# Kernel optimization log

Hardware: AMD Instinct MI355X
Metric: run time of the kernel (lower is better)

Reference implementation:

```python
import jax, jax.numpy as jnp
import numpy as np

B, L, CIN, COUT = 8, 2048, 1024, 1024


def setup_inputs() -> dict:
    key = jax.random.key(0)
    ks = jax.random.split(key, 13)
    s_in = 1.0 / np.sqrt(CIN)
    s_out = 1.0 / np.sqrt(COUT)
    return {
        "query": jax.random.normal(ks[0], (B, L, CIN), jnp.float32),
        "key": jax.random.normal(ks[1], (B, L, CIN), jnp.float32),
        "value": jax.random.normal(ks[2], (B, L, CIN), jnp.float32),
        "Wq": jax.random.uniform(ks[3], (COUT, CIN), jnp.float32, -s_in, s_in),
        "bq": jax.random.uniform(ks[4], (COUT,), jnp.float32, -s_in, s_in),
        "Wk": jax.random.uniform(ks[5], (COUT, CIN), jnp.float32, -s_in, s_in),
        "bk": jax.random.uniform(ks[6], (COUT,), jnp.float32, -s_in, s_in),
        "Wv": jax.random.uniform(ks[7], (COUT, CIN), jnp.float32, -s_in, s_in),
        "bv": jax.random.uniform(ks[8], (COUT,), jnp.float32, -s_in, s_in),
        "fcq_w": jax.random.uniform(ks[9], (1, COUT), jnp.float32, -s_out, s_out),
        "fcq_b": jax.random.uniform(ks[10], (1,), jnp.float32, -s_out, s_out),
        "fck_w": jax.random.uniform(ks[11], (1, COUT), jnp.float32, -s_out, s_out),
        "fck_b": jax.random.uniform(ks[12], (1,), jnp.float32, -s_out, s_out),
    }


def reference(query, key, value, Wq, bq, Wk, bk, Wv, bv, fcq_w, fcq_b, fck_w, fck_b):
    # Linear projections (torch Linear: x @ W^T + b)
    w_query = jnp.einsum('blc,oc->blo', query, Wq) + bq   # [B, Lq, COUT]
    w_key = jnp.einsum('blc,oc->blo', key, Wk) + bk       # [B, Lk, COUT]
    w_value = jnp.einsum('blc,oc->blo', value, Wv) + bv   # [B, Lk, COUT]
    # Scalar scores per position, then outer-sum -> [B, Lq, Lk]
    fc_query = jnp.einsum('blo,xo->blx', w_query, fcq_w) + fcq_b  # [B, Lq, 1]
    fc_key = jnp.einsum('blo,xo->blx', w_key, fck_w) + fck_b      # [B, Lk, 1]
    attns = fc_query + jnp.swapaxes(fc_key, 1, 2)                 # [B, Lq, Lk]
    attns = jax.nn.softmax(attns, axis=-1)
    # dropout p=0.0 (eval) -> identity
    outputs = jnp.einsum('bqk,bkd->bqd', attns, w_value)          # [B, Lq, COUT]
    # note: original applies activation to attns after bmm but discards it
    return outputs
```

## Files before the change

kernel.cpp:

```cpp
#include <hip/hip_runtime.h>

#define CIN  1024
#define COUT 1024
#define LB   2048
#define BB   8


__global__ __launch_bounds__(256) void k_u(const float* __restrict__ Wk,
                                           const float* __restrict__ fckw,
                                           float* __restrict__ u) {
    __shared__ float4 red[256];
    const float4* Wk4 = (const float4*)Wk;
    int t = threadIdx.x;
    int cc = blockIdx.x & 3;
    int oc = blockIdx.x >> 2;
    int c4 = cc * 64 + (t & 63);
    int w  = t >> 6;
    float4 acc = make_float4(0.f, 0.f, 0.f, 0.f);
    #pragma unroll
    for (int j = 0; j < 16; ++j) {
        int o = oc * 64 + w + j * 4;
        float f = fckw[o];
        float4 a = Wk4[(size_t)o * 256 + c4];
        acc.x += f * a.x; acc.y += f * a.y; acc.z += f * a.z; acc.w += f * a.w;
    }
    red[t] = acc;
    __syncthreads();
    if (t < 64) {
        float4 a = red[t], b = red[t + 64], c = red[t + 128], d = red[t + 192];
        float4 s;
        s.x = a.x + b.x + c.x + d.x;
        s.y = a.y + b.y + c.y + d.y;
        s.z = a.z + b.z + c.z + d.z;
        s.w = a.w + b.w + c.w + d.w;
        float* up = u + (size_t)cc * 256 + t * 4;
        atomicAdd(up + 0, s.x);
        atomicAdd(up + 1, s.y);
        atomicAdd(up + 2, s.z);
        atomicAdd(up + 3, s.w);
    }
}

__global__ __launch_bounds__(256) void k_scores(const float* __restrict__ key,
                                                const float* __restrict__ u,
                                                float* __restrict__ s) {
    __shared__ float su[CIN];
    int tid = threadIdx.x;
    ((float4*)su)[tid] = ((const float4*)u)[tid];
    __syncthreads();
    int wave = tid >> 6, lane = tid & 63;
    int r = blockIdx.x * 4 + wave;
    const float4* row = (const float4*)(key + (size_t)r * CIN);
    const float4* su4 = (const float4*)su;
    float acc = 0.f;
    #pragma unroll
    for (int j = 0; j < 4; ++j) {
        float4 a = row[lane + j * 64];
        float4 b = su4[lane + j * 64];
        acc += a.x * b.x + a.y * b.y + a.z * b.z + a.w * b.w;
    }
    #pragma unroll
    for (int off = 32; off; off >>= 1) acc += __shfl_down(acc, off, 64);
    if (lane == 0) s[r] = acc;
}

__global__ __launch_bounds__(256) void k_softmax(const float* __restrict__ s,
                                                 float* __restrict__ p,
                                                 float* __restrict__ vbar) {
    __shared__ float wred[4];
    int b = blockIdx.x, t = threadIdx.x;
    int wave = t >> 6, lane = t & 63;
    const float4* s4 = (const float4*)(s + (size_t)b * LB);
    float4 v0 = s4[t], v1 = s4[t + 256];
    float m = fmaxf(fmaxf(fmaxf(v0.x, v0.y), fmaxf(v0.z, v0.w)),
                    fmaxf(fmaxf(v1.x, v1.y), fmaxf(v1.z, v1.w)));
    #pragma unroll
    for (int off = 32; off; off >>= 1) m = fmaxf(m, __shfl_down(m, off, 64));
    if (lane == 0) wred[wave] = m;
    __syncthreads();
    m = fmaxf(fmaxf(wred[0], wred[1]), fmaxf(wred[2], wred[3]));
    __syncthreads();
    v0.x = __expf(v0.x - m); v0.y = __expf(v0.y - m);
    v0.z = __expf(v0.z - m); v0.w = __expf(v0.w - m);
    v1.x = __expf(v1.x - m); v1.y = __expf(v1.y - m);
    v1.z = __expf(v1.z - m); v1.w = __expf(v1.w - m);
    float sum = v0.x + v0.y + v0.z + v0.w + v1.x + v1.y + v1.z + v1.w;
    #pragma unroll
    for (int off = 32; off; off >>= 1) sum += __shfl_down(sum, off, 64);
    if (lane == 0) wred[wave] = sum;
    __syncthreads();
    float inv = 1.f / (wred[0] + wred[1] + wred[2] + wred[3]);
    v0.x *= inv; v0.y *= inv; v0.z *= inv; v0.w *= inv;
    v1.x *= inv; v1.y *= inv; v1.z *= inv; v1.w *= inv;
    float4* p4 = (float4*)(p + (size_t)b * LB);
    p4[t] = v0; p4[t + 256] = v1;
    ((float4*)(vbar + (size_t)b * CIN))[t] = make_float4(0.f, 0.f, 0.f, 0.f);
}

__global__ __launch_bounds__(256) void k_vbar(const float* __restrict__ value,
                                              const float* __restrict__ p,
                                              float* __restrict__ vbar) {
    __shared__ float pl[32];
    int t = threadIdx.x;
    int b  = blockIdx.x >> 6;
    int k0 = (blockIdx.x & 63) * 32;
    if (t < 32) pl[t] = p[(size_t)b * LB + k0 + t];
    __syncthreads();
    const float4* v4 = (const float4*)value + ((size_t)b * LB + k0) * 256 + t;
    float4 acc = make_float4(0.f, 0.f, 0.f, 0.f);
    #pragma unroll 8
    for (int k = 0; k < 32; ++k) {
        float pw = pl[k];
        float4 a = v4[(size_t)k * 256];
        acc.x += pw * a.x; acc.y += pw * a.y; acc.z += pw * a.z; acc.w += pw * a.w;
    }
    float* vp = vbar + (size_t)b * CIN + t * 4;
    atomicAdd(vp + 0, acc.x);
    atomicAdd(vp + 1, acc.y);
    atomicAdd(vp + 2, acc.z);
    atomicAdd(vp + 3, acc.w);
}

__global__ __launch_bounds__(256) void k_orow(const float* __restrict__ Wv,
                                              const float* __restrict__ bv,
                                              const float* __restrict__ vbar,
                                              float* __restrict__ orow) {
    __shared__ float sv[CIN];
    int tid = threadIdx.x;
    int r0 = blockIdx.x * 4;
    int b = r0 >> 10;
    ((float4*)sv)[tid] = ((const float4*)(vbar + (size_t)b * CIN))[tid];
    __syncthreads();
    int wave = tid >> 6, lane = tid & 63;
    int r = r0 + wave;
    int d = r & 1023;
    const float4* row = (const float4*)(Wv + (size_t)d * CIN);
    const float4* sv4 = (const float4*)sv;
    float acc = 0.f;
    #pragma unroll
    for (int j = 0; j < 4; ++j) {
        float4 a = row[lane + j * 64];
        float4 v = sv4[lane + j * 64];
        acc += a.x * v.x + a.y * v.y + a.z * v.z + a.w * v.w;
    }
    #pragma unroll
    for (int off = 32; off; off >>= 1) acc += __shfl_down(acc, off, 64);
    if (lane == 0) orow[r] = acc + bv[d];
}

__global__ __launch_bounds__(256) void k_bcast(const float* __restrict__ orow,
                                               float* __restrict__ out) {
    int t = threadIdx.x;
    int b  = blockIdx.x >> 8;
    int q0 = (blockIdx.x & 255) * 8;
    float4 val = ((const float4*)orow)[b * 256 + t];
    float4* out4 = (float4*)out;
    #pragma unroll
    for (int j = 0; j < 8; ++j)
        out4[((size_t)b * LB + q0 + j) * 256 + t] = val;
}

extern "C" void kernel_launch(void* const* d_in, const int* in_sizes, int n_in,
                              void* d_out, int out_size, void* d_ws, size_t ws_size,
                              hipStream_t stream) {
    const float* key   = (const float*)d_in[1];
    const float* value = (const float*)d_in[2];
    const float* Wk    = (const float*)d_in[5];
    const float* Wv    = (const float*)d_in[7];
    const float* bv    = (const float*)d_in[8];
    const float* fckw  = (const float*)d_in[11];

    float* ws   = (float*)d_ws;
    float* u    = ws;
    float* s    = ws + 1024;
    float* p    = ws + 17408;
    float* vbar = ws + 33792;
    float* orow = ws + 41984;
    float* out  = (float*)d_out;

    hipMemsetAsync(u, 0, 1024 * sizeof(float), stream);

    hipLaunchKernelGGL(k_u,       dim3(64),   dim3(256), 0, stream, Wk, fckw, u);
    hipLaunchKernelGGL(k_scores,  dim3(4096), dim3(256), 0, stream, key, u, s);
    hipLaunchKernelGGL(k_softmax, dim3(8),    dim3(256), 0, stream, s, p, vbar);
    hipLaunchKernelGGL(k_vbar,    dim3(512),  dim3(256), 0, stream, value, p, vbar);
    hipLaunchKernelGGL(k_orow,    dim3(2048), dim3(256), 0, stream, Wv, bv, vbar, orow);
    hipLaunchKernelGGL(k_bcast,   dim3(2048), dim3(256), 0, stream, orow, out);
}
```

Baseline: 242.4 us.

## Fuse key scoring, exponentiation and value weighting into one kernel

Merges the score, softmax and weighted-value kernels into a single pass. Each block computes scores for 16 key rows, exponentiates them and immediately accumulates exp-weighted value rows. It keeps an unnormalised numerator and a denominator with atomics, and divides by the denominator inside the output-row kernel. This removes two launches, the tiny 8-block softmax kernel and the round trips of the score and probability buffers. In exchange it drops the max subtraction, so exp overflow is possible if the scores are large.

```diff
diff --git a/kernel.cpp b/kernel.cpp
--- a/kernel.cpp
+++ b/kernel.cpp
@@ -41,95 +41,76 @@
     }
 }
 
-__global__ __launch_bounds__(256) void k_scores(const float* __restrict__ key,
-                                                const float* __restrict__ u,
-                                                float* __restrict__ s) {
+__global__ __launch_bounds__(256) void k_fused(const float* __restrict__ key,
+                                               const float* __restrict__ value,
+                                               const float* __restrict__ u,
+                                               float* __restrict__ num,
+                                               float* __restrict__ den) {
     __shared__ float su[CIN];
-    int tid = threadIdx.x;
-    ((float4*)su)[tid] = ((const float4*)u)[tid];
+    __shared__ float4 sacc[4][256];
+    __shared__ float sden[4];
+    int t = threadIdx.x;
+    ((float4*)su)[t] = ((const float4*)u)[t];
     __syncthreads();
-    int wave = tid >> 6, lane = tid & 63;
-    int r = blockIdx.x * 4 + wave;
-    const float4* row = (const float4*)(key + (size_t)r * CIN);
+    int wave = t >> 6, lane = t & 63;
+    int b  = blockIdx.x >> 7;
+    int k0 = (blockIdx.x & 127) * 16;
     const float4* su4 = (const float4*)su;
-    float acc = 0.f;
+    float4 acc0 = make_float4(0,0,0,0), acc1 = acc0, acc2 = acc0, acc3 = acc0;
+    float dsum = 0.f;
     #pragma unroll
     for (int j = 0; j < 4; ++j) {
-        float4 a = row[lane + j * 64];
-        float4 b = su4[lane + j * 64];
-        acc += a.x * b.x + a.y * b.y + a.z * b.z + a.w * b.w;
+        int k = k0 + j * 4 + wave;
+        const float4* krow = (const float4*)(key + ((size_t)b * LB + k) * CIN);
+        float s = 0.f;
+        #pragma unroll
+        for (int seg = 0; seg < 4; ++seg) {
+            float4 a = krow[lane + seg * 64];
+            float4 uu = su4[lane + seg * 64];
+            s += a.x * uu.x + a.y * uu.y + a.z * uu.z + a.w * uu.w;
+        }
+        #pragma unroll
+        for (int off = 32; off; off >>= 1) s += __shfl_down(s, off, 64);
+        float e = __expf(__shfl(s, 0, 64));
+        dsum += e;
+        const float4* vrow = (const float4*)(value + ((size_t)b * LB + k) * CIN);
+        float4 a;
+        a = vrow[lane];       acc0.x += e*a.x; acc0.y += e*a.y; acc0.z += e*a.z; acc0.w += e*a.w;
+        a = vrow[lane + 64];  acc1.x += e*a.x; acc1.y += e*a.y; acc1.z += e*a.z; acc1.w += e*a.w;
+        a = vrow[lane + 128]; acc2.x += e*a.x; acc2.y += e*a.y; acc2.z += e*a.z; acc2.w += e*a.w;
+        a = vrow[lane + 192]; acc3.x += e*a.x; acc3.y += e*a.y; acc3.z += e*a.z; acc3.w += e*a.w;
     }
-    #pragma unroll
-    for (int off = 32; off; off >>= 1) acc += __shfl_down(acc, off, 64);
-    if (lane == 0) s[r] = acc;
-}
-
-__global__ __launch_bounds__(256) void k_softmax(const float* __restrict__ s,
-                                                 float* __restrict__ p,
-                                                 float* __restrict__ vbar) {
-    __shared__ float wred[4];
-    int b = blockIdx.x, t = threadIdx.x;
-    int wave = t >> 6, lane = t & 63;
-    const float4* s4 = (const float4*)(s + (size_t)b * LB);
-    float4 v0 = s4[t], v1 = s4[t + 256];
-    float m = fmaxf(fmaxf(fmaxf(v0.x, v0.y), fmaxf(v0.z, v0.w)),
-                    fmaxf(fmaxf(v1.x, v1.y), fmaxf(v1.z, v1.w)));
-    #pragma unroll
-    for (int off = 32; off; off >>= 1) m = fmaxf(m, __shfl_down(m, off, 64));
-    if (lane == 0) wred[wave] = m;
+    sacc[wave][lane]       = acc0;
+    sacc[wave][lane + 64]  = acc1;
+    sacc[wave][lane + 128] = acc2;
+    sacc[wave][lane + 192] = acc3;
+    if (lane == 0) sden[wave] = dsum;
     __syncthreads();
-    m = fmaxf(fmaxf(wred[0], wred[1]), fmaxf(wred[2], wred[3]));
-    __syncthreads();
-    v0.x = __expf(v0.x - m); v0.y = __expf(v0.y - m);
-    v0.z = __expf(v0.z - m); v0.w = __expf(v0.w - m);
-    v1.x = __expf(v1.x - m); v1.y = __expf(v1.y - m);
-    v1.z = __expf(v1.z - m); v1.w = __expf(v1.w - m);
-    float sum = v0.x + v0.y + v0.z + v0.w + v1.x + v1.y + v1.z + v1.w;
-    #pragma unroll
-    for (int off = 32; off; off >>= 1) sum += __shfl_down(sum, off, 64);
-    if (lane == 0) wred[wave] = sum;
-    __syncthreads();
-    float inv = 1.f / (wred[0] + wred[1] + wred[2] + wred[3]);
-    v0.x *= inv; v0.y *= inv; v0.z *= inv; v0.w *= inv;
-    v1.x *= inv; v1.y *= inv; v1.z *= inv; v1.w *= inv;
-    float4* p4 = (float4*)(p + (size_t)b * LB);
-    p4[t] = v0; p4[t + 256] = v1;
-    ((float4*)(vbar + (size_t)b * CIN))[t] = make_float4(0.f, 0.f, 0.f, 0.f);
-}
-
-__global__ __launch_bounds__(256) void k_vbar(const float* __restrict__ value,
-                                              const float* __restrict__ p,
-                                              float* __restrict__ vbar) {
-    __shared__ float pl[32];
-    int t = threadIdx.x;
-    int b  = blockIdx.x >> 6;
-    int k0 = (blockIdx.x & 63) * 32;
-    if (t < 32) pl[t] = p[(size_t)b * LB + k0 + t];
-    __syncthreads();
-    const float4* v4 = (const float4*)value + ((size_t)b * LB + k0) * 256 + t;
-    float4 acc = make_float4(0.f, 0.f, 0.f, 0.f);
-    #pragma unroll 8
-    for (int k = 0; k < 32; ++k) {
-        float pw = pl[k];
-        float4 a = v4[(size_t)k * 256];
-        acc.x += pw * a.x; acc.y += pw * a.y; acc.z += pw * a.z; acc.w += pw * a.w;
-    }
-    float* vp = vbar + (size_t)b * CIN + t * 4;
-    atomicAdd(vp + 0, acc.x);
-    atomicAdd(vp + 1, acc.y);
-    atomicAdd(vp + 2, acc.z);
-    atomicAdd(vp + 3, acc.w);
+    float4 a0 = sacc[0][t], a1 = sacc[1][t], a2 = sacc[2][t], a3 = sacc[3][t];
+    float4 s4;
+    s4.x = a0.x + a1.x + a2.x + a3.x;
+    s4.y = a0.y + a1.y + a2.y + a3.y;
+    s4.z = a0.z + a1.z + a2.z + a3.z;
+    s4.w = a0.w + a1.w + a2.w + a3.w;
+    int c = (t >> 6) * 256 + (t & 63) * 4;
+    float* np = num + (size_t)b * CIN + c;
+    atomicAdd(np + 0, s4.x);
+    atomicAdd(np + 1, s4.y);
+    atomicAdd(np + 2, s4.z);
+    atomicAdd(np + 3, s4.w);
+    if (t == 0) atomicAdd(&den[b], sden[0] + sden[1] + sden[2] + sden[3]);
 }
 
 __global__ __launch_bounds__(256) void k_orow(const float* __restrict__ Wv,
                                               const float* __restrict__ bv,
-                                              const float* __restrict__ vbar,
+                                              const float* __restrict__ num,
+                                              const float* __restrict__ den,
                                               float* __restrict__ orow) {
     __shared__ float sv[CIN];
     int tid = threadIdx.x;
     int r0 = blockIdx.x * 4;
     int b = r0 >> 10;
-    ((float4*)sv)[tid] = ((const float4*)(vbar + (size_t)b * CIN))[tid];
+    ((float4*)sv)[tid] = ((const float4*)(num + (size_t)b * CIN))[tid];
     __syncthreads();
     int wave = tid >> 6, lane = tid & 63;
     int r = r0 + wave;
@@ -145,7 +126,7 @@
     }
     #pragma unroll
     for (int off = 32; off; off >>= 1) acc += __shfl_down(acc, off, 64);
-    if (lane == 0) orow[r] = acc + bv[d];
+    if (lane == 0) orow[r] = acc / den[b] + bv[d];
 }
 
 __global__ __launch_bounds__(256) void k_bcast(const float* __restrict__ orow,
@@ -172,18 +153,15 @@
 
     float* ws   = (float*)d_ws;
     float* u    = ws;
-    float* s    = ws + 1024;
-    float* p    = ws + 17408;
-    float* vbar = ws + 33792;
-    float* orow = ws + 41984;
+    float* num  = ws + 1024;
+    float* den  = ws + 9216;
+    float* orow = ws + 9224;
     float* out  = (float*)d_out;
 
-    hipMemsetAsync(u, 0, 1024 * sizeof(float), stream);
+    hipMemsetAsync(ws, 0, 9224 * sizeof(float), stream);
 
-    hipLaunchKernelGGL(k_u,       dim3(64),   dim3(256), 0, stream, Wk, fckw, u);
-    hipLaunchKernelGGL(k_scores,  dim3(4096), dim3(256), 0, stream, key, u, s);
-    hipLaunchKernelGGL(k_softmax, dim3(8),    dim3(256), 0, stream, s, p, vbar);
-    hipLaunchKernelGGL(k_vbar,    dim3(512),  dim3(256), 0, stream, value, p, vbar);
-    hipLaunchKernelGGL(k_orow,    dim3(2048), dim3(256), 0, stream, Wv, bv, vbar, orow);
-    hipLaunchKernelGGL(k_bcast,   dim3(2048), dim3(256), 0, stream, orow, out);
+    hipLaunchKernelGGL(k_u,     dim3(64),   dim3(256), 0, stream, Wk, fckw, u);
+    hipLaunchKernelGGL(k_fused, dim3(1024), dim3(256), 0, stream, key, value, u, num, den);
+    hipLaunchKernelGGL(k_orow,  dim3(2048), dim3(256), 0, stream, Wv, bv, num, den, orow);
+    hipLaunchKernelGGL(k_bcast, dim3(2048), dim3(256), 0, stream, orow, out);
 }
```

Result: no change. 241.2 us (-0.5%).
